# Kernel optimization log

Hardware: AMD Instinct MI355X
Metric: run time of the kernel (lower is better)

The kernel has to match this reference:

```python
import jax, jax.numpy as jnp
import numpy as np

NUM_OBJ = 512   # batch_size(8) * objects_per_scene(64)
K = 16          # parts per object
N = NUM_OBJ * K # total part nodes = 8192
P = 512         # points per part
E = NUM_OBJ * K * (K - 1)  # 122880 directed intra-object edges


def setup_inputs() -> dict:
    key = jax.random.key(0)
    ks = jax.random.split(key, 16)

    def w(k, shape, fan_in):
        return jax.random.normal(k, shape, jnp.float32) / np.sqrt(fan_in)

    inp = {}
    inp["pcls_arr"] = jax.random.normal(ks[0], (N, P, 6), jnp.float32)
    # PointNetfeat pointwise convs (6->64->128->256), BN affine params
    inp["W1"] = w(ks[1], (6, 64), 6);     inp["b1"] = jnp.zeros(64);  inp["g1"] = jnp.ones(64);  inp["bt1"] = jnp.zeros(64)
    inp["W2"] = w(ks[2], (64, 128), 64);  inp["b2"] = jnp.zeros(128); inp["g2"] = jnp.ones(128); inp["bt2"] = jnp.zeros(128)
    inp["W3"] = w(ks[3], (128, 256), 128); inp["b3"] = jnp.zeros(256); inp["g3"] = jnp.ones(256); inp["bt3"] = jnp.zeros(256)
    # object_embedding Linear(256->256)
    inp["We"] = w(ks[4], (256, 256), 256); inp["be"] = jnp.zeros(256)
    # two GCN layers (256->256->256)
    inp["Wg1"] = w(ks[5], (256, 256), 256); inp["bg1"] = jnp.zeros(256)
    inp["Wg2"] = w(ks[6], (256, 256), 256); inp["bg2"] = jnp.zeros(256)
    # connectivity head: Linear(512->256), Linear(256->256), Linear(256->1)
    inp["Wc1"] = w(ks[7], (512, 256), 512); inp["bc1"] = jnp.zeros(256)
    inp["Wc2"] = w(ks[8], (256, 256), 256); inp["bc2"] = jnp.zeros(256)
    inp["Wc3"] = w(ks[9], (256, 1), 256);   inp["bc3"] = jnp.zeros(1)
    # dense intra-object directed edges (i != j), matching the nested-loop construction
    ii, jj = np.meshgrid(np.arange(K), np.arange(K), indexing="ij")
    m = ii != jj
    i_loc, j_loc = ii[m], jj[m]            # [K*(K-1)] local pair indices, row-major order
    base = (np.arange(NUM_OBJ) * K)[:, None]
    inp["edge_src"] = jnp.asarray((base + i_loc[None, :]).reshape(-1), jnp.int32)
    inp["edge_dst"] = jnp.asarray((base + j_loc[None, :]).reshape(-1), jnp.int32)
    inp["edge_obj"] = jnp.asarray(np.repeat(np.arange(NUM_OBJ), K * (K - 1)), jnp.int32)
    inp["edge_i"]   = jnp.asarray(np.tile(i_loc, NUM_OBJ), jnp.int32)
    inp["edge_j"]   = jnp.asarray(np.tile(j_loc, NUM_OBJ), jnp.int32)
    return inp


def _bn(x, g, bt):
    # eval-mode BatchNorm with running_mean=0, running_var=1 -> per-channel affine
    return x * g + bt


def _gcn_layer(x, W, b, edge_src, edge_dst):
    # GCNConv with self-loops and symmetric deg^{-1/2} normalization
    xw = x @ W                                               # [N, C]
    deg = jax.ops.segment_sum(jnp.ones(E, x.dtype), edge_dst, num_segments=N) + 1.0
    dinv = deg ** -0.5
    norm = dinv[edge_src] * dinv[edge_dst]                   # [E]
    agg = jax.ops.segment_sum(xw[edge_src] * norm[:, None], edge_dst, num_segments=N)
    agg = agg + xw * (1.0 / deg)[:, None]                    # self-loop term
    return agg + b


def reference(pcls_arr, W1, b1, g1, bt1, W2, b2, g2, bt2, W3, b3, g3, bt3,
              We, be, Wg1, bg1, Wg2, bg2, Wc1, bc1, Wc2, bc2, Wc3, bc3,
              edge_src, edge_dst, edge_obj, edge_i, edge_j):
    # PointNetfeat: pointwise MLP over points, max-pool -> [N, 256]
    h = jax.nn.relu(_bn(pcls_arr @ W1 + b1, g1, bt1))        # [N, P, 64]
    h = jax.nn.relu(_bn(h @ W2 + b2, g2, bt2))               # [N, P, 128]
    h = _bn(h @ W3 + b3, g3, bt3)                            # [N, P, 256]
    feat = jnp.max(h, axis=1)                                # [N, 256]
    emb = feat @ We + be                                     # object_embedding

    # MultiGCN: gcn -> relu -> gcn
    x = jax.nn.relu(_gcn_layer(emb, Wg1, bg1, edge_src, edge_dst))
    x = _gcn_layer(x, Wg2, bg2, edge_src, edge_dst)          # [N, 256]

    # gather parent/child embeddings, concat, connectivity MLP, tanh
    pair = jnp.concatenate([x[edge_src], x[edge_dst]], axis=1)  # [E, 512]
    c = jax.nn.relu(pair @ Wc1 + bc1)
    c = jax.nn.relu(c @ Wc2 + bc2)
    c = jnp.tanh((c @ Wc3 + bc3)[:, 0])                      # [E]

    # scatter edge scores into per-object KxK matrices (zero diagonal)
    out = jnp.zeros((NUM_OBJ, K, K), c.dtype).at[edge_obj, edge_i, edge_j].set(c)
    return out
```

## Files before the change

### kernel.cpp

```cpp
#include <hip/hip_runtime.h>
#include <stdint.h>
#include <stddef.h>


typedef short bf16x8 __attribute__((ext_vector_type(8)));
typedef short bf16x4 __attribute__((ext_vector_type(4)));
typedef float f32x4  __attribute__((ext_vector_type(4)));

#define WT1_OFF   0u
#define WT2_OFF   4096u
#define WT3_OFF   20480u
#define B1F_OFF   86016u
#define B2F_OFF   86272u
#define B3F_OFF   86784u
#define FSUM_OFF  87808u
#define WC1S_OFF  612096u

__device__ __forceinline__ unsigned short f2bf(float f) {
  union { float f; unsigned u; } v; v.f = f;
  unsigned r = v.u + 0x7fffu + ((v.u >> 16) & 1u);
  return (unsigned short)(r >> 16);
}

__device__ __forceinline__ bf16x4 pack_relu4(f32x4 d) {
  bf16x4 o;
  o.x = (short)f2bf(fmaxf(d.x, 0.f));
  o.y = (short)f2bf(fmaxf(d.y, 0.f));
  o.z = (short)f2bf(fmaxf(d.z, 0.f));
  o.w = (short)f2bf(fmaxf(d.w, 0.f));
  return o;
}

__global__ void prep_kernel(
    const float* __restrict__ W1, const float* __restrict__ b1,
    const float* __restrict__ g1, const float* __restrict__ bt1,
    const float* __restrict__ W2, const float* __restrict__ b2,
    const float* __restrict__ g2, const float* __restrict__ bt2,
    const float* __restrict__ W3, const float* __restrict__ b3,
    const float* __restrict__ g3, const float* __restrict__ bt3,
    const float* __restrict__ Wc1, unsigned char* __restrict__ ws)
{
  unsigned short* wt1 = (unsigned short*)(ws + WT1_OFF);
  unsigned short* wt2 = (unsigned short*)(ws + WT2_OFF);
  unsigned short* wt3 = (unsigned short*)(ws + WT3_OFF);
  float* b1f  = (float*)(ws + B1F_OFF);
  float* b2f  = (float*)(ws + B2F_OFF);
  float* b3f  = (float*)(ws + B3F_OFF);
  float* wc1s = (float*)(ws + WC1S_OFF);

  int i = blockIdx.x * 256 + threadIdx.x;
  if (i < 2048) { int o = i >> 5, c = i & 31;
    wt1[i] = f2bf(c < 6 ? W1[c*64 + o] * g1[o] : 0.f); return; }
  i -= 2048;
  if (i < 8192) { int o = i >> 6, c = i & 63;
    wt2[i] = f2bf(W2[c*128 + o] * g2[o]); return; }
  i -= 8192;
  if (i < 32768) { int o = i >> 7, c = i & 127;
    wt3[i] = f2bf(W3[c*256 + o] * g3[o]); return; }
  i -= 32768;
  if (i < 64)  { b1f[i] = b1[i]*g1[i] + bt1[i]; return; }
  i -= 64;
  if (i < 128) { b2f[i] = b2[i]*g2[i] + bt2[i]; return; }
  i -= 128;
  if (i < 256) { b3f[i] = b3[i]*g3[i] + bt3[i]; return; }
  i -= 256;
  if (i < 65536) { wc1s[i] = Wc1[i] + Wc1[i + 65536]; }
}

#define LDSX  0
#define LDSH1 5120
#define LDSH2 14336

__global__ __launch_bounds__(256)
__attribute__((amdgpu_waves_per_eu(2, 2)))
void pointnet_kernel(
    const float* __restrict__ pcls, const unsigned char* __restrict__ ws,
    float* __restrict__ fsum)
{
  __shared__ __align__(16) unsigned short lds[31744];

  const unsigned short* wt1 = (const unsigned short*)(ws + WT1_OFF);
  const unsigned short* wt2 = (const unsigned short*)(ws + WT2_OFF);
  const unsigned short* wt3 = (const unsigned short*)(ws + WT3_OFF);
  const float* b1f = (const float*)(ws + B1F_OFF);
  const float* b2f = (const float*)(ws + B2F_OFF);
  const float* b3f = (const float*)(ws + B3F_OFF);

  const int tid  = threadIdx.x;
  const int w    = tid >> 6;
  const int lane = tid & 63;
  const int l15  = lane & 15;
  const int q    = lane >> 4;
  const int obj  = blockIdx.x;

  bf16x8 af1 = *(const bf16x8*)(wt1 + (16*w + l15)*32 + q*8);
  bf16x8 af2[2][2], af3[4][4];
#pragma unroll
  for (int nt = 0; nt < 2; ++nt)
#pragma unroll
    for (int kf = 0; kf < 2; ++kf)
      af2[nt][kf] = *(const bf16x8*)(wt2 + (32*w + nt*16 + l15)*64 + kf*32 + q*8);
#pragma unroll
  for (int nt = 0; nt < 4; ++nt)
#pragma unroll
    for (int kf = 0; kf < 4; ++kf)
      af3[nt][kf] = *(const bf16x8*)(wt3 + (64*w + nt*16 + l15)*128 + kf*32 + q*8);

  const f32x4 bias1 = *(const f32x4*)(b1f + 16*w + q*4);
  f32x4 bias2[2], bias3[4];
#pragma unroll
  for (int nt = 0; nt < 2; ++nt) bias2[nt] = *(const f32x4*)(b2f + 32*w + nt*16 + q*4);
#pragma unroll
  for (int nt = 0; nt < 4; ++nt) bias3[nt] = *(const f32x4*)(b3f + 64*w + nt*16 + q*4);

  int soff[3];
#pragma unroll
  for (int j = 0; j < 3; ++j) {
    int i = tid + 256*j; int p = i / 6; int c = i - 6*p;
    soff[j] = LDSX + p*40 + c;
  }

  for (int i = tid; i < 5120; i += 256) lds[LDSX + i] = 0;
  __syncthreads();

  const float* pbase = pcls + (size_t)obj * 49152;
#pragma unroll
  for (int j = 0; j < 3; ++j)
    lds[soff[j]] = f2bf(pbase[tid + 256*j]);
  __syncthreads();

  f32x4 macc[4];
  float sacc[4][4];
#pragma unroll
  for (int nt = 0; nt < 4; ++nt) {
    macc[nt] = (f32x4){-3e38f, -3e38f, -3e38f, -3e38f};
#pragma unroll
    for (int r = 0; r < 4; ++r) sacc[nt][r] = 0.f;
  }

  for (int cg = 0; cg < 64; ++cg) {
#pragma unroll
    for (int pt = 0; pt < 8; ++pt) {
      bf16x8 b = *(const bf16x8*)(&lds[LDSX + (pt*16 + l15)*40 + q*8]);
      f32x4 d = bias1;
      d = __builtin_amdgcn_mfma_f32_16x16x32_bf16(af1, b, d, 0, 0, 0);
      *(bf16x4*)(&lds[LDSH1 + (pt*16 + l15)*72 + 16*w + q*4]) = pack_relu4(d);
    }
    __syncthreads();

    float pf[3];
    const int havenext = (cg < 63);
    if (havenext) {
#pragma unroll
      for (int j = 0; j < 3; ++j) pf[j] = pbase[(cg + 1)*768 + tid + 256*j];
    }

#pragma unroll
    for (int pt = 0; pt < 8; ++pt) {
      bf16x8 b0 = *(const bf16x8*)(&lds[LDSH1 + (pt*16 + l15)*72 + q*8]);
      bf16x8 b1v = *(const bf16x8*)(&lds[LDSH1 + (pt*16 + l15)*72 + 32 + q*8]);
#pragma unroll
      for (int nt = 0; nt < 2; ++nt) {
        f32x4 d = bias2[nt];
        d = __builtin_amdgcn_mfma_f32_16x16x32_bf16(af2[nt][0], b0, d, 0, 0, 0);
        d = __builtin_amdgcn_mfma_f32_16x16x32_bf16(af2[nt][1], b1v, d, 0, 0, 0);
        *(bf16x4*)(&lds[LDSH2 + (pt*16 + l15)*136 + 32*w + nt*16 + q*4]) = pack_relu4(d);
      }
    }
    if (havenext) {
#pragma unroll
      for (int j = 0; j < 3; ++j) lds[soff[j]] = f2bf(pf[j]);
    }
    __syncthreads();

#pragma unroll
    for (int pt = 0; pt < 8; ++pt) {
      bf16x8 b[4];
#pragma unroll
      for (int kf = 0; kf < 4; ++kf)
        b[kf] = *(const bf16x8*)(&lds[LDSH2 + (pt*16 + l15)*136 + kf*32 + q*8]);
#pragma unroll
      for (int nt = 0; nt < 4; ++nt) {
        f32x4 d = bias3[nt];
#pragma unroll
        for (int kf = 0; kf < 4; ++kf)
          d = __builtin_amdgcn_mfma_f32_16x16x32_bf16(af3[nt][kf], b[kf], d, 0, 0, 0);
#pragma unroll
        for (int r = 0; r < 4; ++r)
          macc[nt][r] = fmaxf(macc[nt][r], d[r]);
      }
    }
    if ((cg & 3) == 3) {
#pragma unroll
      for (int nt = 0; nt < 4; ++nt) {
#pragma unroll
        for (int r = 0; r < 4; ++r) {
          float v = macc[nt][r];
          v = fmaxf(v, __shfl_xor(v, 1));
          v = fmaxf(v, __shfl_xor(v, 2));
          v = fmaxf(v, __shfl_xor(v, 4));
          v = fmaxf(v, __shfl_xor(v, 8));
          sacc[nt][r] += v;
        }
        macc[nt] = (f32x4){-3e38f, -3e38f, -3e38f, -3e38f};
      }
    }
    __syncthreads();
  }

#pragma unroll
  for (int r = 0; r < 4; ++r) {
    if (l15 == r) {
#pragma unroll
      for (int nt = 0; nt < 4; ++nt)
        fsum[obj*256 + 64*w + nt*16 + q*4 + r] = sacc[nt][r];
    }
  }
}

__global__ __launch_bounds__(256) void objmlp_kernel(
    const float* __restrict__ We,  const float* __restrict__ be,
    const float* __restrict__ Wg1, const float* __restrict__ bg1,
    const float* __restrict__ Wg2, const float* __restrict__ bg2,
    const float* __restrict__ bc1,
    const float* __restrict__ Wc2, const float* __restrict__ bc2,
    const float* __restrict__ Wc3, const float* __restrict__ bc3,
    const unsigned char* __restrict__ ws, float* __restrict__ out)
{
  const float* fsum = (const float*)(ws + FSUM_OFF);
  const float* Wc1s = (const float*)(ws + WC1S_OFF);
  __shared__ float bufA[256], bufB[256], red[4], cval_s;
  const int t = threadIdx.x, obj = blockIdx.x;

  bufA[t] = fsum[obj*256 + t];
  __syncthreads();
  float acc = 0.f;
#pragma unroll 8
  for (int c = 0; c < 256; ++c) acc += bufA[c] * We[c*256 + t];
  bufB[t] = acc + 16.f * be[t];
  __syncthreads();
  acc = 0.f;
#pragma unroll 8
  for (int c = 0; c < 256; ++c) acc += bufB[c] * Wg1[c*256 + t];
  bufA[t] = fmaxf(acc * 0.0625f + bg1[t], 0.f);
  __syncthreads();
  acc = 0.f;
#pragma unroll 8
  for (int c = 0; c < 256; ++c) acc += bufA[c] * Wg2[c*256 + t];
  bufB[t] = acc + bg2[t];
  __syncthreads();
  acc = 0.f;
#pragma unroll 8
  for (int c = 0; c < 256; ++c) acc += bufB[c] * Wc1s[c*256 + t];
  bufA[t] = fmaxf(acc + bc1[t], 0.f);
  __syncthreads();
  acc = 0.f;
#pragma unroll 8
  for (int c = 0; c < 256; ++c) acc += bufA[c] * Wc2[c*256 + t];
  float h2v = fmaxf(acc + bc2[t], 0.f);

  float part = h2v * Wc3[t];
#pragma unroll
  for (int off = 1; off < 64; off <<= 1) part += __shfl_xor(part, off);
  if ((t & 63) == 0) red[t >> 6] = part;
  __syncthreads();
  if (t == 0) cval_s = tanhf(red[0] + red[1] + red[2] + red[3] + bc3[0]);
  __syncthreads();
  const float cv = cval_s;
  out[obj*256 + t] = ((t >> 4) == (t & 15)) ? 0.f : cv;
}

extern "C" void kernel_launch(void* const* d_in, const int* in_sizes, int n_in,
                              void* d_out, int out_size, void* d_ws, size_t ws_size,
                              hipStream_t stream) {
  const float* pcls = (const float*)d_in[0];
  const float* W1 = (const float*)d_in[1];  const float* b1 = (const float*)d_in[2];
  const float* g1 = (const float*)d_in[3];  const float* bt1 = (const float*)d_in[4];
  const float* W2 = (const float*)d_in[5];  const float* b2 = (const float*)d_in[6];
  const float* g2 = (const float*)d_in[7];  const float* bt2 = (const float*)d_in[8];
  const float* W3 = (const float*)d_in[9];  const float* b3 = (const float*)d_in[10];
  const float* g3 = (const float*)d_in[11]; const float* bt3 = (const float*)d_in[12];
  const float* We = (const float*)d_in[13]; const float* be = (const float*)d_in[14];
  const float* Wg1 = (const float*)d_in[15]; const float* bg1 = (const float*)d_in[16];
  const float* Wg2 = (const float*)d_in[17]; const float* bg2 = (const float*)d_in[18];
  const float* Wc1 = (const float*)d_in[19]; const float* bc1 = (const float*)d_in[20];
  const float* Wc2 = (const float*)d_in[21]; const float* bc2 = (const float*)d_in[22];
  const float* Wc3 = (const float*)d_in[23]; const float* bc3 = (const float*)d_in[24];
  unsigned char* ws = (unsigned char*)d_ws;
  float* out = (float*)d_out;

  prep_kernel<<<426, 256, 0, stream>>>(W1, b1, g1, bt1, W2, b2, g2, bt2,
                                       W3, b3, g3, bt3, Wc1, ws);
  pointnet_kernel<<<512, 256, 0, stream>>>(pcls, ws, (float*)(ws + FSUM_OFF));
  objmlp_kernel<<<512, 256, 0, stream>>>(We, be, Wg1, bg1, Wg2, bg2, bc1,
                                         Wc2, bc2, Wc3, bc3, ws, out);
}
```

Baseline: 558.8 us.

## Split each pointnet object across two blocks with atomic partial-sum reduction

```diff
diff --git a/kernel.cpp b/kernel.cpp
--- a/kernel.cpp
+++ b/kernel.cpp
@@ -1,4 +1,5 @@
 #include <hip/hip_runtime.h>
+#include <hip/hip_bf16.h>
 #include <stdint.h>
 #include <stddef.h>
 
@@ -23,12 +24,11 @@
 }
 
 __device__ __forceinline__ bf16x4 pack_relu4(f32x4 d) {
-  bf16x4 o;
-  o.x = (short)f2bf(fmaxf(d.x, 0.f));
-  o.y = (short)f2bf(fmaxf(d.y, 0.f));
-  o.z = (short)f2bf(fmaxf(d.z, 0.f));
-  o.w = (short)f2bf(fmaxf(d.w, 0.f));
-  return o;
+  __hip_bfloat162 lo = __float22bfloat162_rn(make_float2(fmaxf(d.x, 0.f), fmaxf(d.y, 0.f)));
+  __hip_bfloat162 hi = __float22bfloat162_rn(make_float2(fmaxf(d.z, 0.f), fmaxf(d.w, 0.f)));
+  union { bf16x4 v; __hip_bfloat162 h[2]; } u;
+  u.h[0] = lo; u.h[1] = hi;
+  return u.v;
 }
 
 __global__ void prep_kernel(
@@ -47,10 +47,13 @@
   float* b2f  = (float*)(ws + B2F_OFF);
   float* b3f  = (float*)(ws + B3F_OFF);
   float* wc1s = (float*)(ws + WC1S_OFF);
+  float* fsum = (float*)(ws + FSUM_OFF);
 
   int i = blockIdx.x * 256 + threadIdx.x;
   if (i < 2048) { int o = i >> 5, c = i & 31;
-    wt1[i] = f2bf(c < 6 ? W1[c*64 + o] * g1[o] : 0.f); return; }
+    float v = (c < 6) ? W1[c*64 + o] * g1[o]
+            : (c == 6 ? (b1[o]*g1[o] + bt1[o]) : 0.f);
+    wt1[i] = f2bf(v); return; }
   i -= 2048;
   if (i < 8192) { int o = i >> 6, c = i & 63;
     wt2[i] = f2bf(W2[c*128 + o] * g2[o]); return; }
@@ -64,25 +67,26 @@
   i -= 128;
   if (i < 256) { b3f[i] = b3[i]*g3[i] + bt3[i]; return; }
   i -= 256;
-  if (i < 65536) { wc1s[i] = Wc1[i] + Wc1[i + 65536]; }
+  if (i < 65536) { wc1s[i] = Wc1[i] + Wc1[i + 65536]; return; }
+  i -= 65536;
+  if (i < 131072) { fsum[i] = 0.f; }
 }
 
 #define LDSX  0
-#define LDSH1 5120
-#define LDSH2 14336
+#define LDSH1 2560
+#define LDSH2 7168
 
 __global__ __launch_bounds__(256)
-__attribute__((amdgpu_waves_per_eu(2, 2)))
+__attribute__((amdgpu_waves_per_eu(3, 4)))
 void pointnet_kernel(
     const float* __restrict__ pcls, const unsigned char* __restrict__ ws,
     float* __restrict__ fsum)
 {
-  __shared__ __align__(16) unsigned short lds[31744];
+  __shared__ __align__(16) unsigned short lds[15872];
 
   const unsigned short* wt1 = (const unsigned short*)(ws + WT1_OFF);
   const unsigned short* wt2 = (const unsigned short*)(ws + WT2_OFF);
   const unsigned short* wt3 = (const unsigned short*)(ws + WT3_OFF);
-  const float* b1f = (const float*)(ws + B1F_OFF);
   const float* b2f = (const float*)(ws + B2F_OFF);
   const float* b3f = (const float*)(ws + B3F_OFF);
 
@@ -91,7 +95,7 @@
   const int lane = tid & 63;
   const int l15  = lane & 15;
   const int q    = lane >> 4;
-  const int obj  = blockIdx.x;
+  const int obj  = blockIdx.x >> 1;
 
   bf16x8 af1 = *(const bf16x8*)(wt1 + (16*w + l15)*32 + q*8);
   bf16x8 af2[2][2], af3[4][4];
@@ -106,27 +110,26 @@
     for (int kf = 0; kf < 4; ++kf)
       af3[nt][kf] = *(const bf16x8*)(wt3 + (64*w + nt*16 + l15)*128 + kf*32 + q*8);
 
-  const f32x4 bias1 = *(const f32x4*)(b1f + 16*w + q*4);
   f32x4 bias2[2], bias3[4];
 #pragma unroll
   for (int nt = 0; nt < 2; ++nt) bias2[nt] = *(const f32x4*)(b2f + 32*w + nt*16 + q*4);
 #pragma unroll
   for (int nt = 0; nt < 4; ++nt) bias3[nt] = *(const f32x4*)(b3f + 64*w + nt*16 + q*4);
 
-  int soff[3];
-#pragma unroll
-  for (int j = 0; j < 3; ++j) {
-    int i = tid + 256*j; int p = i / 6; int c = i - 6*p;
-    soff[j] = LDSX + p*40 + c;
-  }
-
-  for (int i = tid; i < 5120; i += 256) lds[LDSX + i] = 0;
-  __syncthreads();
-
-  const float* pbase = pcls + (size_t)obj * 49152;
-#pragma unroll
-  for (int j = 0; j < 3; ++j)
-    lds[soff[j]] = f2bf(pbase[tid + 256*j]);
+  const int i1v = tid < 128;
+  int p0 = tid / 6,          c0 = tid - 6*p0;
+  int p1 = (256 + tid) / 6,  c1 = (256 + tid) - 6*p1;
+  const int soff0 = LDSX + p0*40 + c0;
+  const int soff1 = LDSX + p1*40 + c1;
+
+  for (int i = tid; i < 2560; i += 256) lds[i] = 0;
+  __syncthreads();
+  if (tid < 64) lds[LDSX + tid*40 + 6] = 0x3F80;
+  __syncthreads();
+
+  const float* pbase = pcls + (size_t)blockIdx.x * 24576;
+  lds[soff0] = f2bf(pbase[tid]);
+  if (i1v) lds[soff1] = f2bf(pbase[256 + tid]);
   __syncthreads();
 
   f32x4 macc[4];
@@ -140,23 +143,23 @@
 
   for (int cg = 0; cg < 64; ++cg) {
 #pragma unroll
-    for (int pt = 0; pt < 8; ++pt) {
+    for (int pt = 0; pt < 4; ++pt) {
       bf16x8 b = *(const bf16x8*)(&lds[LDSX + (pt*16 + l15)*40 + q*8]);
-      f32x4 d = bias1;
+      f32x4 d = {0.f, 0.f, 0.f, 0.f};
       d = __builtin_amdgcn_mfma_f32_16x16x32_bf16(af1, b, d, 0, 0, 0);
       *(bf16x4*)(&lds[LDSH1 + (pt*16 + l15)*72 + 16*w + q*4]) = pack_relu4(d);
     }
     __syncthreads();
 
-    float pf[3];
+    float pf0, pf1;
     const int havenext = (cg < 63);
     if (havenext) {
-#pragma unroll
-      for (int j = 0; j < 3; ++j) pf[j] = pbase[(cg + 1)*768 + tid + 256*j];
-    }
-
-#pragma unroll
-    for (int pt = 0; pt < 8; ++pt) {
+      pf0 = pbase[(cg + 1)*384 + tid];
+      if (i1v) pf1 = pbase[(cg + 1)*384 + 256 + tid];
+    }
+
+#pragma unroll
+    for (int pt = 0; pt < 4; ++pt) {
       bf16x8 b0 = *(const bf16x8*)(&lds[LDSH1 + (pt*16 + l15)*72 + q*8]);
       bf16x8 b1v = *(const bf16x8*)(&lds[LDSH1 + (pt*16 + l15)*72 + 32 + q*8]);
 #pragma unroll
@@ -168,13 +171,13 @@
       }
     }
     if (havenext) {
-#pragma unroll
-      for (int j = 0; j < 3; ++j) lds[soff[j]] = f2bf(pf[j]);
+      lds[soff0] = f2bf(pf0);
+      if (i1v) lds[soff1] = f2bf(pf1);
     }
     __syncthreads();
 
 #pragma unroll
-    for (int pt = 0; pt < 8; ++pt) {
+    for (int pt = 0; pt < 4; ++pt) {
       bf16x8 b[4];
 #pragma unroll
       for (int kf = 0; kf < 4; ++kf)
@@ -190,7 +193,7 @@
           macc[nt][r] = fmaxf(macc[nt][r], d[r]);
       }
     }
-    if ((cg & 3) == 3) {
+    if ((cg & 7) == 7) {
 #pragma unroll
       for (int nt = 0; nt < 4; ++nt) {
 #pragma unroll
@@ -213,7 +216,7 @@
     if (l15 == r) {
 #pragma unroll
       for (int nt = 0; nt < 4; ++nt)
-        fsum[obj*256 + 64*w + nt*16 + q*4 + r] = sacc[nt][r];
+        atomicAdd(&fsum[obj*256 + 64*w + nt*16 + q*4 + r], sacc[nt][r]);
     }
   }
 }
@@ -289,9 +292,9 @@
   unsigned char* ws = (unsigned char*)d_ws;
   float* out = (float*)d_out;
 
-  prep_kernel<<<426, 256, 0, stream>>>(W1, b1, g1, bt1, W2, b2, g2, bt2,
+  prep_kernel<<<938, 256, 0, stream>>>(W1, b1, g1, bt1, W2, b2, g2, bt2,
                                        W3, b3, g3, bt3, Wc1, ws);
-  pointnet_kernel<<<512, 256, 0, stream>>>(pcls, ws, (float*)(ws + FSUM_OFF));
+  pointnet_kernel<<<1024, 256, 0, stream>>>(pcls, ws, (float*)(ws + FSUM_OFF));
   objmlp_kernel<<<512, 256, 0, stream>>>(We, be, Wg1, bg1, Wg2, bg2, bc1,
                                          Wc2, bc2, Wc3, bc3, ws, out);
 }
```

After: 825.8 us. +47.8%, slower.
